# Performance work log

Hardware: AMD Instinct MI355X
Metric: run time of the kernel (lower is better)

The kernel has to match this reference:

```python
import jax, jax.numpy as jnp
import numpy as np

# Hyperparameters matching init_kwargs
IN_CH = 64
OUT_CH = 128
KERNEL = (3, 3)
STRIDE = (1, 1)
PADDING = 'SAME'
K_ORDER = 3          # spline order
G_INTERVALS = 3      # grid intervals
GRID_MIN, GRID_MAX = -1.0, 1.0
N_BASIS = G_INTERVALS + K_ORDER  # basis functions per input = 6
PATCH_DIM = IN_CH * KERNEL[0] * KERNEL[1]  # 576


def _grid():
    # Extended uniform knot vector: G + 2k + 1 knots
    h = (GRID_MAX - GRID_MIN) / G_INTERVALS
    return jnp.arange(-K_ORDER, G_INTERVALS + K_ORDER + 1, dtype=jnp.float32) * h + GRID_MIN


def _b_splines(x):
    # x: [N, n_in] -> bases: [N, n_in, G + k]
    grid = _grid()  # [G + 2k + 1]
    xe = x[..., None]  # [N, n_in, 1]
    bases = ((xe >= grid[:-1]) & (xe < grid[1:])).astype(x.dtype)  # order-0, [N, n_in, G+2k]
    for p in range(1, K_ORDER + 1):
        left = (xe - grid[: -(p + 1)]) / (grid[p:-1] - grid[: -(p + 1)]) * bases[..., :-1]
        right = (grid[p + 1:] - xe) / (grid[p + 1:] - grid[1:-p]) * bases[..., 1:]
        bases = left + right
    return bases  # [N, n_in, G + k]


def setup_inputs() -> dict:
    key = jax.random.key(0)
    k0, k1, k2, k3 = jax.random.split(key, 4)
    x = jax.random.normal(k0, (8, 64, 64, IN_CH), dtype=jnp.float32)
    base_w = jax.random.normal(k1, (OUT_CH, PATCH_DIM), dtype=jnp.float32) * 0.05
    spline_w = jax.random.normal(k2, (OUT_CH, PATCH_DIM, N_BASIS), dtype=jnp.float32) * 0.05
    bias = jax.random.normal(k3, (OUT_CH,), dtype=jnp.float32) * 0.05
    return {'x': x, 'base_w': base_w, 'spline_w': spline_w, 'bias': bias}


def reference(x, base_w, spline_w, bias):
    batch = x.shape[0]
    dn = ('NHWC', 'HWIO', 'NHWC')
    patches = jax.lax.conv_general_dilated_patches(
        lhs=x, filter_shape=KERNEL, window_strides=STRIDE, padding=PADDING,
        dimension_numbers=dn)  # [B, H, W, patch_dim]
    out_spatial = patches.shape[1:-1]
    p = patches.reshape(-1, PATCH_DIM)  # [N, patch_dim]
    # EfficientKAN: residual (silu) branch + spline branch + bias
    base_out = jax.nn.silu(p) @ base_w.T                      # [N, out]
    bases = _b_splines(p)                                      # [N, patch_dim, G+k]
    spline_out = jnp.einsum('nig,oig->no', bases, spline_w)    # [N, out]
    y = base_out + spline_out + bias
    return y.reshape(batch, *out_spatial, OUT_CH)
```

## Files before the change

kernel.cpp:

```cpp
#include <hip/hip_runtime.h>

typedef __attribute__((ext_vector_type(8))) short short8;
typedef __attribute__((ext_vector_type(16))) float f32x16;

#define FT2_SHORTS (512u * 4356u * 8u)
#define PLANE16    4356

__device__ __forceinline__ unsigned short f2bf(float x) {
    union { float f; unsigned u; } v; v.f = x;
    unsigned r = v.u + 0x7FFFu + ((v.u >> 16) & 1u);
    return (unsigned short)(r >> 16);
}

__device__ __forceinline__ void feat8(float p, unsigned short* uf) {
    float e   = __expf(-p);
    float sig = 1.f / (1.f + e);
    uf[0] = f2bf(p * sig);
    float u  = p * 1.5f + 4.5f;
    float fj = floorf(u);
    int   j0 = (int)fj;
    float t  = u - fj;
    bool  inr = (u >= 0.f) && (u < 9.f);
    float t2 = t * t, t3 = t2 * t;
    const float c16 = 1.f / 6.f;
    float r0 = t3 * c16;
    float r1 = (-3.f * t3 + 3.f * t2 + 3.f * t + 1.f) * c16;
    float r2 = (3.f * t3 - 6.f * t2 + 4.f) * c16;
    float s1 = 1.f - t;
    float r3 = s1 * s1 * s1 * c16;
#pragma unroll
    for (int g = 0; g < 6; ++g) {
        int r = j0 - g;
        float v = (r == 0) ? r0 : ((r == 1) ? r1 : ((r == 2) ? r2 : ((r == 3) ? r3 : 0.f)));
        uf[1 + g] = f2bf(inr ? v : 0.f);
    }
    uf[7] = 0;
}

__global__ __launch_bounds__(256)
void prep_all(const float* __restrict__ x,
              const float* __restrict__ bw, const float* __restrict__ sw,
              unsigned short* __restrict__ ft, unsigned short* __restrict__ wt) {
    const int blk = blockIdx.x;
    const int tid = threadIdx.x;

    if (tid < 144) {
        int idx = blk * 144 + tid;
        int o = idx / 576;
        int i = idx - o * 576;
        union { unsigned short u[8]; uint4 v; } pk;
        pk.u[0] = f2bf(bw[o * 576 + i]);
        const float* s = sw + (size_t)(o * 576 + i) * 6;
#pragma unroll
        for (int f = 0; f < 6; ++f) pk.u[1 + f] = f2bf(s[f]);
        pk.u[7] = 0;
        *(uint4*)(wt + ((size_t)i * 1024 + o * 8)) = pk.v;
    }

    {
        short8 pad = { 0, 0, (short)0x3CAB, (short)0x3EF5,
                       (short)0x3EF5, (short)0x3CAB, 0, 0 };
        for (int t = tid; t < 260; t += 256) {
            int yy, xx;
            if (t < 66)       { yy = 0;       xx = t; }
            else if (t < 132) { yy = 65;      xx = t - 66; }
            else if (t < 196) { yy = t - 131; xx = 0; }
            else              { yy = t - 195; xx = 65; }
            ((short8*)ft)[blk * PLANE16 + yy * 66 + xx] = pad;
        }
    }

    __shared__ float Xl[64 * 65];
    const int b = blk >> 6, y = blk & 63;
    const float* xl = x + (size_t)blk * 4096;
    for (int f4 = tid; f4 < 1024; f4 += 256) {
        float4 v = ((const float4*)xl)[f4];
        int xx = f4 >> 4, c4 = (f4 & 15) << 2;
        float* d = &Xl[xx * 65 + c4];
        d[0] = v.x; d[1] = v.y; d[2] = v.z; d[3] = v.w;
    }
    __syncthreads();
    const int xx = tid & 63;
    const int cw = tid >> 6;
#pragma unroll 4
    for (int p = 0; p < 16; ++p) {
        int c = cw + (p << 2);
        float pv = Xl[xx * 65 + c];
        union { unsigned short u[8]; uint4 v; } pk;
        feat8(pv, pk.u);
        size_t o16 = (size_t)(c * 8 + b) * PLANE16 + (y + 1) * 66 + (xx + 1);
        *(uint4*)(ft + (o16 << 3)) = pk.v;
    }
}

#define DZ2 2230272u

#define MFMA4(P)                                                                      \
    acc00 = __builtin_amdgcn_mfma_f32_32x32x16_bf16(P##a0, P##b0, acc00, 0, 0, 0);    \
    acc01 = __builtin_amdgcn_mfma_f32_32x32x16_bf16(P##a0, P##b1, acc01, 0, 0, 0);    \
    acc10 = __builtin_amdgcn_mfma_f32_32x32x16_bf16(P##a1, P##b0, acc10, 0, 0, 0);    \
    acc11 = __builtin_amdgcn_mfma_f32_32x32x16_bf16(P##a1, P##b1, acc11, 0, 0, 0);

#define ISS(P, CAX, S2)                                                               \
    P##a0 = *(const short8*)(ftc + (CAX) + aoff##S2);                                 \
    P##a1 = *(const short8*)(ftc + (CAX) + aoff##S2 + 512);                           \
    P##b0 = *(const short8*)(wtc + bv);                                               \
    P##b1 = *(const short8*)(wtc + bv + 512);                                         \
    bv += 4096u;

#define PAIR(SA, SB, CAX, CAN, LAST)                                                  \
    MFMA4(SA) ISS(SA, CAX, 2)                                                         \
    MFMA4(SB) ISS(SB, CAX, 3)                                                         \
    MFMA4(SA) ISS(SA, CAX, 4)                                                         \
    MFMA4(SB) ISS(SB, CAX, 5)                                                         \
    MFMA4(SA) ISS(SA, CAX, 6)                                                         \
    MFMA4(SB) ISS(SB, CAX, 7)                                                         \
    MFMA4(SA) ISS(SA, CAX, 8)                                                         \
    bv += 36864u;                         \
    MFMA4(SB) if (!(LAST)) { ISS(SB, CAN, 0) }                                        \
    MFMA4(SA) if (!(LAST)) { ISS(SA, CAN, 1) }

#define MKAOFF(S)                                                                     \
    int aoff##S; {                                                                    \
        int t_ = 2 * (S) + h; int co_ = (t_ >= 9) ? 1 : 0; int j_ = t_ - 9 * co_;     \
        int kh_ = (j_ * 11) >> 5; int kw_ = j_ - kh_ * 3;                             \
        aoff##S = co_ * (8 * PLANE16 * 16) + (kh_ * 66 + kw_) * 16;                   \
    }

#define DUMPA(base_, A_)                                                              \
    {   float4* s4 = (float4*)(red + (base_));                                        \
        _Pragma("unroll")                                                             \
        for (int c = 0; c < 4; ++c)                                                   \
            s4[c * 64 + lane] = make_float4(A_[4*c], A_[4*c+1], A_[4*c+2], A_[4*c+3]); }
#define ADDA(base_, A_)                                                               \
    {   const float4* s4 = (const float4*)(red + (base_));                            \
        _Pragma("unroll")                                                             \
        for (int c = 0; c < 4; ++c) {                                                 \
            float4 rv = s4[c * 64 + lane];                                            \
            A_[4*c] += rv.x; A_[4*c+1] += rv.y; A_[4*c+2] += rv.z; A_[4*c+3] += rv.w; } }

__global__ __launch_bounds__(512, 2)
void convkan_gemm(const unsigned short* __restrict__ ft,
                  const unsigned short* __restrict__ wt,
                  const float* __restrict__ bias,
                  float* __restrict__ out) {
    __shared__ float red[16384];

    const int tid  = threadIdx.x;
    const int blk  = blockIdx.x;
    const int mb   = ((blk & 7) << 5) | (blk >> 3);
    const int lane = tid & 63;
    const int wave = tid >> 6;
    const int kq   = wave >> 2;
    const int mh   = (wave >> 1) & 1;
    const int nh   = wave & 1;
    const int l32  = lane & 31;
    const int h    = lane >> 5;

    const int b  = mb >> 5;
    const int y0 = (mb & 31) << 1;

    const char* ftc = (const char*)ft;
    const char* wtc = (const char*)wt;

    MKAOFF(0) MKAOFF(1) MKAOFF(2) MKAOFF(3) MKAOFF(4)
    MKAOFF(5) MKAOFF(6) MKAOFF(7) MKAOFF(8)

    unsigned cax = ((unsigned)((16 * kq + b) * PLANE16 + (y0 + mh) * 66 + l32)) << 4;
    unsigned can = cax + DZ2;
    unsigned bv  = ((unsigned)(18 * kq + h) << 11) + (((unsigned)(nh * 64 + l32)) << 4);

    f32x16 acc00, acc01, acc10, acc11;
#pragma unroll
    for (int e = 0; e < 16; ++e) { acc00[e] = 0.f; acc01[e] = 0.f; acc10[e] = 0.f; acc11[e] = 0.f; }

    short8 Aa0, Aa1, Ab0, Ab1;
    short8 Ba0, Ba1, Bb0, Bb1;

    ISS(A, cax, 0)
    ISS(B, cax, 1)

    for (int w = 0; w < 7; ++w) {
        PAIR(A, B, cax, can, 0) cax = can; can += DZ2;
        PAIR(B, A, cax, can, 0) cax = can; can += DZ2;
    }
    PAIR(A, B, cax, can, 0) cax = can;
    PAIR(B, A, cax, cax, 1)

    __syncthreads();
    const int grp = mh * 2 + nh;

    if (kq == 1) {
        DUMPA(grp * 4096,        acc00); DUMPA(grp * 4096 + 1024, acc01);
        DUMPA(grp * 4096 + 2048, acc10); DUMPA(grp * 4096 + 3072, acc11);
    }
    __syncthreads();
    if (kq == 0) {
        ADDA(grp * 4096,        acc00); ADDA(grp * 4096 + 1024, acc01);
        ADDA(grp * 4096 + 2048, acc10); ADDA(grp * 4096 + 3072, acc11);

        const int ncol = nh * 64 + l32;
        const float bv0 = bias[ncol];
        const float bv1 = bias[ncol + 32];
        const int prow = mb * 128 + mh * 64;
#pragma unroll
        for (int r = 0; r < 16; ++r) {
            int mrow = (r & 3) + ((r >> 2) << 3) + 4 * h;
            float* p = out + (size_t)(prow + mrow) * 128 + ncol;
            p[0]  = acc00[r] + bv0;
            p[32] = acc01[r] + bv1;
            float* p2 = out + (size_t)(prow + 32 + mrow) * 128 + ncol;
            p2[0]  = acc10[r] + bv0;
            p2[32] = acc11[r] + bv1;
        }
    }
}

extern "C" void kernel_launch(void* const* d_in, const int* in_sizes, int n_in,
                              void* d_out, int out_size, void* d_ws, size_t ws_size,
                              hipStream_t stream) {
    (void)in_sizes; (void)n_in; (void)ws_size; (void)out_size;
    const float* x        = (const float*)d_in[0];
    const float* base_w   = (const float*)d_in[1];
    const float* spline_w = (const float*)d_in[2];
    const float* bias     = (const float*)d_in[3];
    float* out = (float*)d_out;

    unsigned short* ft = (unsigned short*)d_ws;
    unsigned short* wt = ft + FT2_SHORTS;

    hipLaunchKernelGGL(prep_all, dim3(512), dim3(256), 0, stream,
                       x, base_w, spline_w, ft, wt);

    hipLaunchKernelGGL(convkan_gemm, dim3(256), dim3(512), 0, stream,
                       ft, wt, bias, out);
}
```

Before: 141.4 us.

## Split GEMM K dimension across three wave groups instead of two

```diff
diff --git a/kernel.cpp b/kernel.cpp
--- a/kernel.cpp
+++ b/kernel.cpp
@@ -93,7 +93,14 @@
     }
 }
 
-#define DZ2 2230272u
+#define DZ3 3345408u
+
+__host__ __device__ constexpr int AOC(int t) {
+    return ((t >= 9) ? 557568 : 0)
+         + (((((t - ((t >= 9) ? 9 : 0)) * 11) >> 5) * 66
+            + ((t - ((t >= 9) ? 9 : 0)) - ((((t - ((t >= 9) ? 9 : 0)) * 11) >> 5) * 3))) * 16);
+}
+#define AOFF(S2) (h ? AOC(2 * (S2) + 1) : AOC(2 * (S2)))
 
 #define MFMA4(P)                                                                      \
     acc00 = __builtin_amdgcn_mfma_f32_32x32x16_bf16(P##a0, P##b0, acc00, 0, 0, 0);    \
@@ -101,12 +108,13 @@
     acc10 = __builtin_amdgcn_mfma_f32_32x32x16_bf16(P##a1, P##b0, acc10, 0, 0, 0);    \
     acc11 = __builtin_amdgcn_mfma_f32_32x32x16_bf16(P##a1, P##b1, acc11, 0, 0, 0);
 
-#define ISS(P, CAX, S2)                                                               \
-    P##a0 = *(const short8*)(ftc + (CAX) + aoff##S2);                                 \
-    P##a1 = *(const short8*)(ftc + (CAX) + aoff##S2 + 512);                           \
+#define ISS(P, CAX, S2) {                                                             \
+    const int ao_ = AOFF(S2);                                                         \
+    P##a0 = *(const short8*)(ftc + (CAX) + ao_);                                      \
+    P##a1 = *(const short8*)(ftc + (CAX) + ao_ + 512);                                \
     P##b0 = *(const short8*)(wtc + bv);                                               \
     P##b1 = *(const short8*)(wtc + bv + 512);                                         \
-    bv += 4096u;
+    bv += 4096u; }
 
 #define PAIR(SA, SB, CAX, CAN, LAST)                                                  \
     MFMA4(SA) ISS(SA, CAX, 2)                                                         \
@@ -116,16 +124,9 @@
     MFMA4(SA) ISS(SA, CAX, 6)                                                         \
     MFMA4(SB) ISS(SB, CAX, 7)                                                         \
     MFMA4(SA) ISS(SA, CAX, 8)                                                         \
-    bv += 36864u;                         \
+    bv += 73728u;                        \
     MFMA4(SB) if (!(LAST)) { ISS(SB, CAN, 0) }                                        \
     MFMA4(SA) if (!(LAST)) { ISS(SA, CAN, 1) }
-
-#define MKAOFF(S)                                                                     \
-    int aoff##S; {                                                                    \
-        int t_ = 2 * (S) + h; int co_ = (t_ >= 9) ? 1 : 0; int j_ = t_ - 9 * co_;     \
-        int kh_ = (j_ * 11) >> 5; int kw_ = j_ - kh_ * 3;                             \
-        aoff##S = co_ * (8 * PLANE16 * 16) + (kh_ * 66 + kw_) * 16;                   \
-    }
 
 #define DUMPA(base_, A_)                                                              \
     {   float4* s4 = (float4*)(red + (base_));                                        \
@@ -139,12 +140,12 @@
             float4 rv = s4[c * 64 + lane];                                            \
             A_[4*c] += rv.x; A_[4*c+1] += rv.y; A_[4*c+2] += rv.z; A_[4*c+3] += rv.w; } }
 
-__global__ __launch_bounds__(512, 2)
+__global__ __launch_bounds__(768, 3)
 void convkan_gemm(const unsigned short* __restrict__ ft,
                   const unsigned short* __restrict__ wt,
                   const float* __restrict__ bias,
                   float* __restrict__ out) {
-    __shared__ float red[16384];
+    extern __shared__ float red[];
 
     const int tid  = threadIdx.x;
     const int blk  = blockIdx.x;
@@ -163,11 +164,7 @@
     const char* ftc = (const char*)ft;
     const char* wtc = (const char*)wt;
 
-    MKAOFF(0) MKAOFF(1) MKAOFF(2) MKAOFF(3) MKAOFF(4)
-    MKAOFF(5) MKAOFF(6) MKAOFF(7) MKAOFF(8)
-
     unsigned cax = ((unsigned)((16 * kq + b) * PLANE16 + (y0 + mh) * 66 + l32)) << 4;
-    unsigned can = cax + DZ2;
     unsigned bv  = ((unsigned)(18 * kq + h) << 11) + (((unsigned)(nh * 64 + l32)) << 4);
 
     f32x16 acc00, acc01, acc10, acc11;
@@ -180,24 +177,34 @@
     ISS(A, cax, 0)
     ISS(B, cax, 1)
 
-    for (int w = 0; w < 7; ++w) {
-        PAIR(A, B, cax, can, 0) cax = can; can += DZ2;
-        PAIR(B, A, cax, can, 0) cax = can; can += DZ2;
-    }
-    PAIR(A, B, cax, can, 0) cax = can;
-    PAIR(B, A, cax, cax, 1)
+    for (int w = 0; w < 4; ++w) {
+        PAIR(A, B, cax, cax + DZ3, 0) cax += DZ3;
+        PAIR(B, A, cax, cax + DZ3, 0) cax += DZ3;
+    }
+    if (kq < 2) {
+        PAIR(A, B, cax, cax + DZ3, 0) cax += DZ3;
+        PAIR(B, A, cax, cax + DZ3, 0) cax += DZ3;
+        PAIR(A, B, cax, cax, 1)
+    } else {
+        PAIR(A, B, cax, cax + DZ3, 0) cax += DZ3;
+        PAIR(B, A, cax, cax, 1)
+    }
 
     __syncthreads();
     const int grp = mh * 2 + nh;
 
-    if (kq == 1) {
-        DUMPA(grp * 4096,        acc00); DUMPA(grp * 4096 + 1024, acc01);
-        DUMPA(grp * 4096 + 2048, acc10); DUMPA(grp * 4096 + 3072, acc11);
+    if (kq != 0) {
+        const int rb = ((kq - 1) * 4 + grp) * 4096;
+        DUMPA(rb,        acc00); DUMPA(rb + 1024, acc01);
+        DUMPA(rb + 2048, acc10); DUMPA(rb + 3072, acc11);
     }
     __syncthreads();
     if (kq == 0) {
-        ADDA(grp * 4096,        acc00); ADDA(grp * 4096 + 1024, acc01);
-        ADDA(grp * 4096 + 2048, acc10); ADDA(grp * 4096 + 3072, acc11);
+        const int r1 = grp * 4096, r2 = (4 + grp) * 4096;
+        ADDA(r1,        acc00); ADDA(r1 + 1024, acc01);
+        ADDA(r1 + 2048, acc10); ADDA(r1 + 3072, acc11);
+        ADDA(r2,        acc00); ADDA(r2 + 1024, acc01);
+        ADDA(r2 + 2048, acc10); ADDA(r2 + 3072, acc11);
 
         const int ncol = nh * 64 + l32;
         const float bv0 = bias[ncol];
@@ -232,6 +239,9 @@
     hipLaunchKernelGGL(prep_all, dim3(512), dim3(256), 0, stream,
                        x, base_w, spline_w, ft, wt);
 
-    hipLaunchKernelGGL(convkan_gemm, dim3(256), dim3(512), 0, stream,
+    const int shmem = 32768 * 4;
+    (void)hipFuncSetAttribute((const void*)convkan_gemm,
+                              hipFuncAttributeMaxDynamicSharedMemorySize, shmem);
+    hipLaunchKernelGGL(convkan_gemm, dim3(256), dim3(768), shmem, stream,
                        ft, wt, bias, out);
 }
```

After: 199.5 us. +41.1%, slower.
